# Kernel tuning notes

Measured on AMD Instinct MI355X. Metric: run time of the kernel, lower is better.

The kernel has to match this reference:

```python
import jax, jax.numpy as jnp
import numpy as np

BNK, L, DIN, DOUT, NREL = 1280, 64, 512, 256, 40

def setup_inputs() -> dict:
    key = jax.random.key(0)
    ks = jax.random.split(key, 10)
    rep = jax.random.normal(ks[0], (BNK, L, DIN), dtype=jnp.float32)
    # adj_arc_in[..., 0] = flattened sentence index, adj_arc_in[..., 1] = head token position
    sent = jnp.broadcast_to(jnp.arange(BNK, dtype=jnp.int64)[:, None], (BNK, L))
    head = jax.random.randint(ks[1], (BNK, L), 0, L, dtype=jnp.int64)
    adj_arc_in = jnp.stack([sent, head], axis=-1)  # [BNK, L, 2]
    adj_lab_in = jax.random.randint(ks[2], (BNK, L), 0, NREL, dtype=jnp.int64)
    adj_mask_in = (jax.random.uniform(ks[3], (BNK, L)) < 0.9).astype(jnp.float32)
    adj_mask_loop = jnp.ones((BNK, L), dtype=jnp.float32)
    mask = jnp.ones((BNK, L), dtype=jnp.float32)
    # parameters (xavier-ish init)
    W_in = jax.random.normal(ks[4], (DIN, DOUT), dtype=jnp.float32) * (2.0 / (DIN + DOUT)) ** 0.5
    b_in = jnp.zeros((NREL, DOUT), dtype=jnp.float32)
    W_gate_in = jax.random.uniform(ks[5], (DIN, 1), dtype=jnp.float32)
    b_gate_in = jnp.ones((NREL, 1), dtype=jnp.float32)
    W_self = jax.random.normal(ks[6], (DIN, DOUT), dtype=jnp.float32) * (2.0 / (DIN + DOUT)) ** 0.5
    W_gate_self = jax.random.uniform(ks[7], (DIN, 1), dtype=jnp.float32)
    return {"rep": rep, "adj_mask_in": adj_mask_in, "adj_mask_loop": adj_mask_loop,
            "mask": mask, "W_in": W_in, "b_in": b_in, "W_gate_in": W_gate_in,
            "b_gate_in": b_gate_in, "W_self": W_self, "W_gate_self": W_gate_self,
            "adj_arc_in": adj_arc_in, "adj_lab_in": adj_lab_in}

def reference(rep, adj_mask_in, adj_mask_loop, mask, W_in, b_in, W_gate_in,
              b_gate_in, W_self, W_gate_self, adj_arc_in, adj_lab_in):
    bnk, l, din = rep.shape
    dout = W_in.shape[1]
    rep_ = rep.reshape(bnk * l, din)                    # [M, Din]
    idx = adj_arc_in[..., 0].reshape(-1) * l + adj_arc_in[..., 1].reshape(-1)  # [M]
    lab = adj_lab_in.reshape(-1)                        # [M]
    # in-arc potential: gather projected head token, add relation-typed bias
    in_pot = (rep_ @ W_in)[idx] + b_in[lab]             # [M, Dout]
    in_gate = (rep_ @ W_gate_in)[idx, 0] + b_gate_in[lab, 0]  # [M]
    # self-loop potential
    self_pot = rep_ @ W_self                            # [M, Dout]
    self_gate = (rep_ @ W_gate_self)[:, 0]              # [M]
    pots = jnp.stack([in_pot, self_pot], axis=1)        # [M, 2, Dout]
    gates = jnp.stack([in_gate, self_gate], axis=1)     # [M, 2]
    msoft = jnp.stack([adj_mask_in.reshape(-1), adj_mask_loop.reshape(-1)], axis=1)  # [M, 2]
    # original multiplies by mask_soft twice: potentials * mask_soft * (sigmoid(gate) * mask_soft)
    w = jax.nn.sigmoid(gates) * msoft * msoft           # [M, 2]
    res = jax.nn.relu(jnp.einsum('mdk,md->mk', pots, w))  # [M, Dout]
    res = res.reshape(bnk, l, dout) * mask.reshape(bnk, l)[..., None]
    return res
```

## Files before the change

### kernel.cpp

```cpp
#include <hip/hip_runtime.h>


#define BNK   1280
#define LTOK  64
#define DIN   512
#define DOUT  256
#define TPB   512
#define PSTR  264

#define SMEM_BYTES 77568

typedef __attribute__((ext_vector_type(4))) float f32x4;
typedef __attribute__((ext_vector_type(8))) short s16x8;

__device__ __forceinline__ unsigned short f2bf(float f) {
  unsigned u = __float_as_uint(f);
  unsigned r = (u + 0x7FFFu + ((u >> 16) & 1u)) >> 16;
  return (unsigned short)r;
}
__device__ __forceinline__ float bf2f(unsigned short h) {
  return __uint_as_float(((unsigned)h) << 16);
}
__device__ __forceinline__ float sigmoidf_(float x) {
  return 1.0f / (1.0f + __expf(-x));
}

__global__ __launch_bounds__(256) void wprep_kernel(const float* __restrict__ W_in,
                                                    const float* __restrict__ W_self,
                                                    unsigned short* __restrict__ Wt) {
  __shared__ float tile[32][33];
  const int t  = threadIdx.x;
  const int c0 = (blockIdx.x & 15) * 32;
  const int k0 = (blockIdx.x >> 4) * 32;
  const float* src = (c0 < DOUT) ? W_in : W_self;
  const int cadj   = (c0 < DOUT) ? c0 : (c0 - DOUT);
  {
    const int kk = t >> 3;
    const int cc = (t & 7) * 4;
    const float4 v = *(const float4*)(src + (size_t)(k0 + kk) * DOUT + cadj + cc);
    tile[kk][cc + 0] = v.x; tile[kk][cc + 1] = v.y;
    tile[kk][cc + 2] = v.z; tile[kk][cc + 3] = v.w;
  }
  __syncthreads();
  {
    const int cc = t >> 3;
    const int kk = (t & 7) * 4;
    ushort4 o;
    o.x = f2bf(tile[kk + 0][cc]); o.y = f2bf(tile[kk + 1][cc]);
    o.z = f2bf(tile[kk + 2][cc]); o.w = f2bf(tile[kk + 3][cc]);
    *(ushort4*)(Wt + (size_t)(c0 + cc) * DIN + k0 + kk) = o;
  }
}

__global__ __launch_bounds__(TPB, 4) void gcn_kernel(
    const float* __restrict__ rep,
    const float* __restrict__ adj_mask_in,
    const float* __restrict__ adj_mask_loop,
    const float* __restrict__ maskp,
    const float* __restrict__ b_in,
    const float* __restrict__ w_gate_in,
    const float* __restrict__ b_gate_in,
    const float* __restrict__ w_gate_self,
    const int* __restrict__ arc,
    const int* __restrict__ lab,
    const unsigned short* __restrict__ Wt,
    float* __restrict__ out)
{
  __shared__ __align__(16) char smem[SMEM_BYTES];
  unsigned short* As  = (unsigned short*)(smem);
  unsigned short* Pin = (unsigned short*)(smem);
  unsigned short* Psf = (unsigned short*)(smem + 33792);
  float* wgi  = (float*)(smem + 67584);
  float* wgs  = (float*)(smem + 69632);
  float* part = (float*)(smem + 71680);
  float* gld  = (float*)(smem + 75776);
  float* winl = (float*)(smem + 76288);
  float* wsfl = (float*)(smem + 76544);
  float* mskl = (float*)(smem + 76800);
  int*   hdl  = (int*)(smem + 77056);
  int*   lbl  = (int*)(smem + 77312);

  const int b    = blockIdx.x;
  const int t    = threadIdx.x;
  const int wave = t >> 6;
  const int lane = t & 63;
  const int nlo  = lane & 15;
  const int quad = lane >> 4;

  wgi[t] = w_gate_in[t];
  wgs[t] = w_gate_self[t];
  __syncthreads();

  {
    const int r = t >> 3, p = t & 7;
    const float* arow = rep + (size_t)(b * LTOK + r) * DIN;
    float si = 0.f, ss = 0.f;
    #pragma unroll 4
    for (int i = 0; i < 8; ++i) {
      const int kg = p + 8 * i;
      const int kb = kg * 8;
      const float4 v0 = *(const float4*)(arow + kb);
      const float4 v1 = *(const float4*)(arow + kb + 4);
      const float4 g0 = *(const float4*)(wgi + kb);
      const float4 g1 = *(const float4*)(wgi + kb + 4);
      const float4 h0 = *(const float4*)(wgs + kb);
      const float4 h1 = *(const float4*)(wgs + kb + 4);
      si += v0.x*g0.x + v0.y*g0.y + v0.z*g0.z + v0.w*g0.w
          + v1.x*g1.x + v1.y*g1.y + v1.z*g1.z + v1.w*g1.w;
      ss += v0.x*h0.x + v0.y*h0.y + v0.z*h0.z + v0.w*h0.w
          + v1.x*h1.x + v1.y*h1.y + v1.z*h1.z + v1.w*h1.w;
      s16x8 o;
      o[0] = (short)f2bf(v0.x); o[1] = (short)f2bf(v0.y);
      o[2] = (short)f2bf(v0.z); o[3] = (short)f2bf(v0.w);
      o[4] = (short)f2bf(v1.x); o[5] = (short)f2bf(v1.y);
      o[6] = (short)f2bf(v1.z); o[7] = (short)f2bf(v1.w);
      const int u = (kg >> 2) * 256 + (kg & 3) * 64 + (r ^ p);
      *(s16x8*)(As + u * 8) = o;
    }
    part[t * 2 + 0] = si;
    part[t * 2 + 1] = ss;
  }
  __syncthreads();

  if (t < 128) {
    const int r = t >> 1, g = t & 1;
    float s = 0.f;
    #pragma unroll
    for (int p = 0; p < 8; ++p) s += part[(r * 8 + p) * 2 + g];
    gld[r * 2 + g] = s;
  }

  f32x4 acc[4][4];
  #pragma unroll
  for (int i = 0; i < 4; ++i)
    #pragma unroll
    for (int j = 0; j < 4; ++j) {
      f32x4 z = {0.f, 0.f, 0.f, 0.f};
      acc[i][j] = z;
    }

  const unsigned short* aeven = As + (quad * 64 + (nlo ^ quad)) * 8;
  const unsigned short* aodd  = As + (quad * 64 + (nlo ^ (quad + 4))) * 8;
  const unsigned short* wb = Wt + (size_t)(wave * 64 + nlo) * DIN + quad * 8;

  #pragma unroll
  for (int kc = 0; kc < 16; ++kc) {
    const unsigned short* ab = ((kc & 1) ? aodd : aeven) + kc * 2048;
    const unsigned short* wk = wb + kc * 32;
    s16x8 af[4], bf[4];
    #pragma unroll
    for (int mt = 0; mt < 4; ++mt)
      af[mt] = *(const s16x8*)(ab + mt * 128);
    #pragma unroll
    for (int nt = 0; nt < 4; ++nt)
      bf[nt] = *(const s16x8*)(wk + nt * 16 * DIN);
    #pragma unroll
    for (int nt = 0; nt < 4; ++nt)
      #pragma unroll
      for (int mt = 0; mt < 4; ++mt)
        acc[mt][nt] = __builtin_amdgcn_mfma_f32_16x16x32_bf16(af[mt], bf[nt], acc[mt][nt], 0, 0, 0);
  }

  __syncthreads();

  if (t < LTOK) {
    const int m  = b * LTOK + t;
    const int hd = arc[2 * m + 1];
    const int lb = lab[m];
    const float am = adj_mask_in[m];
    const float al = adj_mask_loop[m];
    winl[t] = sigmoidf_(gld[hd * 2 + 0] + b_gate_in[lb]) * am * am;
    wsfl[t] = sigmoidf_(gld[t * 2 + 1]) * al * al;
    mskl[t] = maskp[m];
    hdl[t]  = hd;
    lbl[t]  = lb;
  }

  {
    unsigned short* dst = (wave < 4) ? Pin : Psf;
    const int cb = (wave & 3) * 64;
    #pragma unroll
    for (int mt = 0; mt < 4; ++mt)
      #pragma unroll
      for (int nt = 0; nt < 4; ++nt)
        #pragma unroll
        for (int rr = 0; rr < 4; ++rr) {
          const int row = mt * 16 + quad * 4 + rr;
          const int col = cb + nt * 16 + nlo;
          dst[row * PSTR + col] = f2bf(acc[mt][nt][rr]);
        }
  }
  __syncthreads();

  #pragma unroll
  for (int i = 0; i < 8; ++i) {
    const int row = i * 8 + wave;
    const int cl  = (t & 63) * 4;
    const int hd  = hdl[row];
    const int lb  = lbl[row];
    const float wi = winl[row], ws = wsfl[row], mk = mskl[row];
    const float4  bi = *(const float4*)(b_in + lb * DOUT + cl);
    const ushort4 pi = *(const ushort4*)(Pin + hd * PSTR + cl);
    const ushort4 ps = *(const ushort4*)(Psf + row * PSTR + cl);
    float4 v;
    v.x = (bf2f(pi.x) + bi.x) * wi + bf2f(ps.x) * ws;
    v.y = (bf2f(pi.y) + bi.y) * wi + bf2f(ps.y) * ws;
    v.z = (bf2f(pi.z) + bi.z) * wi + bf2f(ps.z) * ws;
    v.w = (bf2f(pi.w) + bi.w) * wi + bf2f(ps.w) * ws;
    v.x = fmaxf(v.x, 0.f) * mk; v.y = fmaxf(v.y, 0.f) * mk;
    v.z = fmaxf(v.z, 0.f) * mk; v.w = fmaxf(v.w, 0.f) * mk;
    *(float4*)(out + (size_t)(b * LTOK + row) * DOUT + cl) = v;
  }
}

extern "C" void kernel_launch(void* const* d_in, const int* in_sizes, int n_in,
                              void* d_out, int out_size, void* d_ws, size_t ws_size,
                              hipStream_t stream) {
  const float* rep           = (const float*)d_in[0];
  const float* adj_mask_in   = (const float*)d_in[1];
  const float* adj_mask_loop = (const float*)d_in[2];
  const float* mask          = (const float*)d_in[3];
  const float* W_in          = (const float*)d_in[4];
  const float* b_in          = (const float*)d_in[5];
  const float* W_gate_in     = (const float*)d_in[6];
  const float* b_gate_in     = (const float*)d_in[7];
  const float* W_self        = (const float*)d_in[8];
  const float* W_gate_self   = (const float*)d_in[9];
  const int*   arc           = (const int*)d_in[10];
  const int*   lab           = (const int*)d_in[11];
  float* out = (float*)d_out;
  unsigned short* Wt = (unsigned short*)d_ws;

  wprep_kernel<<<256, 256, 0, stream>>>(W_in, W_self, Wt);
  gcn_kernel<<<BNK, TPB, 0, stream>>>(rep, adj_mask_in, adj_mask_loop, mask, b_in,
                                      W_gate_in, b_gate_in, W_gate_self, arc, lab, Wt, out);
}
```

Measured before the change: 357.6 us.

## Double block size to 16 waves, prefetch W fragments, shuffle-reduce gate dots

Raises threads per block from 512 to 1024, so each of 16 waves computes a 64x32 output slice instead of 64x64. This halves accumulator registers and adds more latency-hiding waves per block. The gate dot-products are now reduced with wavefront xor shuffles instead of a shared-memory partial buffer, which removes one barrier and frees that LDS. W fragments from global memory are prefetched two k-steps ahead in a triple-buffered register ring, and MFMA sections are bracketed with s_setprio. The risks are that launch_bounds(1024,4) may force register spilling or lower occupancy, and that the A fragments are now read by twice as many waves.

```diff
diff --git a/kernel.cpp b/kernel.cpp
--- a/kernel.cpp
+++ b/kernel.cpp
@@ -5,10 +5,10 @@
 #define LTOK  64
 #define DIN   512
 #define DOUT  256
-#define TPB   512
+#define TPB   1024
 #define PSTR  264
 
-#define SMEM_BYTES 77568
+#define SMEM_BYTES 73472
 
 typedef __attribute__((ext_vector_type(4))) float f32x4;
 typedef __attribute__((ext_vector_type(8))) short s16x8;
@@ -72,32 +72,33 @@
   unsigned short* Psf = (unsigned short*)(smem + 33792);
   float* wgi  = (float*)(smem + 67584);
   float* wgs  = (float*)(smem + 69632);
-  float* part = (float*)(smem + 71680);
-  float* gld  = (float*)(smem + 75776);
-  float* winl = (float*)(smem + 76288);
-  float* wsfl = (float*)(smem + 76544);
-  float* mskl = (float*)(smem + 76800);
-  int*   hdl  = (int*)(smem + 77056);
-  int*   lbl  = (int*)(smem + 77312);
+  float* gld  = (float*)(smem + 71680);
+  float* winl = (float*)(smem + 72192);
+  float* wsfl = (float*)(smem + 72448);
+  float* mskl = (float*)(smem + 72704);
+  int*   hdl  = (int*)(smem + 72960);
+  int*   lbl  = (int*)(smem + 73216);
 
   const int b    = blockIdx.x;
   const int t    = threadIdx.x;
-  const int wave = t >> 6;
+  const int w    = t >> 6;
   const int lane = t & 63;
   const int nlo  = lane & 15;
   const int quad = lane >> 4;
 
-  wgi[t] = w_gate_in[t];
-  wgs[t] = w_gate_self[t];
-  __syncthreads();
-
-  {
-    const int r = t >> 3, p = t & 7;
+  if (t < DIN) {
+    wgi[t] = w_gate_in[t];
+    wgs[t] = w_gate_self[t];
+  }
+  __syncthreads();
+
+  {
+    const int r = t >> 4, p = t & 15;
     const float* arow = rep + (size_t)(b * LTOK + r) * DIN;
     float si = 0.f, ss = 0.f;
-    #pragma unroll 4
-    for (int i = 0; i < 8; ++i) {
-      const int kg = p + 8 * i;
+    #pragma unroll
+    for (int i = 0; i < 4; ++i) {
+      const int kg = p + 16 * i;
       const int kb = kg * 8;
       const float4 v0 = *(const float4*)(arow + kb);
       const float4 v1 = *(const float4*)(arow + kb + 4);
@@ -114,51 +115,59 @@
       o[2] = (short)f2bf(v0.z); o[3] = (short)f2bf(v0.w);
       o[4] = (short)f2bf(v1.x); o[5] = (short)f2bf(v1.y);
       o[6] = (short)f2bf(v1.z); o[7] = (short)f2bf(v1.w);
-      const int u = (kg >> 2) * 256 + (kg & 3) * 64 + (r ^ p);
+      const int u = ((p >> 2) + 4 * i) * 256 + (p & 3) * 64 + (r ^ (p & 7));
       *(s16x8*)(As + u * 8) = o;
     }
-    part[t * 2 + 0] = si;
-    part[t * 2 + 1] = ss;
-  }
-  __syncthreads();
-
-  if (t < 128) {
-    const int r = t >> 1, g = t & 1;
-    float s = 0.f;
-    #pragma unroll
-    for (int p = 0; p < 8; ++p) s += part[(r * 8 + p) * 2 + g];
-    gld[r * 2 + g] = s;
-  }
-
-  f32x4 acc[4][4];
+    #pragma unroll
+    for (int off = 1; off < 16; off <<= 1) {
+      si += __shfl_xor(si, off, 64);
+      ss += __shfl_xor(ss, off, 64);
+    }
+    if (p == 0) {
+      gld[r * 2 + 0] = si;
+      gld[r * 2 + 1] = ss;
+    }
+  }
+  __syncthreads();
+
+  f32x4 acc[4][2];
   #pragma unroll
   for (int i = 0; i < 4; ++i)
     #pragma unroll
-    for (int j = 0; j < 4; ++j) {
+    for (int j = 0; j < 2; ++j) {
       f32x4 z = {0.f, 0.f, 0.f, 0.f};
       acc[i][j] = z;
     }
 
   const unsigned short* aeven = As + (quad * 64 + (nlo ^ quad)) * 8;
   const unsigned short* aodd  = As + (quad * 64 + (nlo ^ (quad + 4))) * 8;
-  const unsigned short* wb = Wt + (size_t)(wave * 64 + nlo) * DIN + quad * 8;
+  const unsigned short* wb0 = Wt + (size_t)(w * 32 + nlo) * DIN + quad * 8;
+  const unsigned short* wb1 = wb0 + 16 * DIN;
+
+  s16x8 bfr[3][2];
+  bfr[0][0] = *(const s16x8*)(wb0);
+  bfr[0][1] = *(const s16x8*)(wb1);
+  bfr[1][0] = *(const s16x8*)(wb0 + 32);
+  bfr[1][1] = *(const s16x8*)(wb1 + 32);
 
   #pragma unroll
   for (int kc = 0; kc < 16; ++kc) {
+    if (kc + 2 < 16) {
+      bfr[(kc + 2) % 3][0] = *(const s16x8*)(wb0 + (kc + 2) * 32);
+      bfr[(kc + 2) % 3][1] = *(const s16x8*)(wb1 + (kc + 2) * 32);
+    }
     const unsigned short* ab = ((kc & 1) ? aodd : aeven) + kc * 2048;
-    const unsigned short* wk = wb + kc * 32;
-    s16x8 af[4], bf[4];
+    s16x8 af[4];
     #pragma unroll
     for (int mt = 0; mt < 4; ++mt)
       af[mt] = *(const s16x8*)(ab + mt * 128);
-    #pragma unroll
-    for (int nt = 0; nt < 4; ++nt)
-      bf[nt] = *(const s16x8*)(wk + nt * 16 * DIN);
-    #pragma unroll
-    for (int nt = 0; nt < 4; ++nt)
+    __builtin_amdgcn_s_setprio(1);
+    #pragma unroll
+    for (int nt = 0; nt < 2; ++nt)
       #pragma unroll
       for (int mt = 0; mt < 4; ++mt)
-        acc[mt][nt] = __builtin_amdgcn_mfma_f32_16x16x32_bf16(af[mt], bf[nt], acc[mt][nt], 0, 0, 0);
+        acc[mt][nt] = __builtin_amdgcn_mfma_f32_16x16x32_bf16(af[mt], bfr[kc % 3][nt], acc[mt][nt], 0, 0, 0);
+    __builtin_amdgcn_s_setprio(0);
   }
 
   __syncthreads();
@@ -177,12 +186,12 @@
   }
 
   {
-    unsigned short* dst = (wave < 4) ? Pin : Psf;
-    const int cb = (wave & 3) * 64;
+    unsigned short* dst = (w < 8) ? Pin : Psf;
+    const int cb = (w & 7) * 32;
     #pragma unroll
     for (int mt = 0; mt < 4; ++mt)
       #pragma unroll
-      for (int nt = 0; nt < 4; ++nt)
+      for (int nt = 0; nt < 2; ++nt)
         #pragma unroll
         for (int rr = 0; rr < 4; ++rr) {
           const int row = mt * 16 + quad * 4 + rr;
@@ -193,9 +202,10 @@
   __syncthreads();
 
   #pragma unroll
-  for (int i = 0; i < 8; ++i) {
-    const int row = i * 8 + wave;
-    const int cl  = (t & 63) * 4;
+  for (int i = 0; i < 4; ++i) {
+    const int q   = i * TPB + t;
+    const int row = q >> 6;
+    const int cl  = (q & 63) * 4;
     const int hd  = hdl[row];
     const int lb  = lbl[row];
     const float wi = winl[row], ws = wsfl[row], mk = mskl[row];
```

Measured after the change: 353.0 us. No clear change (-1.3%).
